# Kernel tuning notes

Hardware: AMD Instinct MI355X
Metric: run time of the kernel (lower is better)

## Reference

```python
import jax, jax.numpy as jnp
import numpy as np

B, N, NE = 16, 96, 256
ATOM, EDIM, HID, LAT, HEADS = 128, 16, 128, 128, 4
HD = LAT // HEADS
RBF, CUT, ZEMB, MAXZ = 16, 5.0, 32, 100
MUL0_IN, MUL1_IN = 64, 32      # irreps_node = 64x0e + 32x1o (dim 160)
MUL0_OUT, MUL1_OUT = 32, 16    # out irreps  = 32x0e + 16x1o (dim 80)
NODE_DIM = MUL0_IN + 3 * MUL1_IN
OUT_DIM = MUL0_OUT + 3 * MUL1_OUT
E_ATT = 1024
WNUM = MUL0_IN*MUL0_OUT + MUL0_IN*MUL1_OUT + MUL1_IN*MUL1_OUT + MUL1_IN*MUL0_OUT  # 4608


def _mlp3(x, w1, b1, w2, b2, w3, b3):
    x = jax.nn.silu(x @ w1 + b1)
    x = jax.nn.silu(x @ w2 + b2)
    return x @ w3 + b3


def setup_inputs() -> dict:
    key = jax.random.key(0)
    ks = jax.random.split(key, 40)
    s = 0.05  # scale params so deep MLP activations stay numerically sane
    d = {}
    d['h'] = jax.random.normal(ks[0], (B, N, ATOM), jnp.float32)
    d['h_full'] = jax.random.normal(ks[1], (B, N, NODE_DIM), jnp.float32)
    d['e_feat'] = jax.random.normal(ks[2], (NE, EDIM), jnp.float32)
    d['att_dist'] = jax.random.uniform(ks[3], (E_ATT,), jnp.float32)
    d['att_vec'] = jax.random.normal(ks[4], (E_ATT, 3), jnp.float32)
    d['z_emb_table'] = jax.random.normal(ks[5], (MAXZ + 1, ZEMB), jnp.float32) * s
    d['rw1'] = jax.random.normal(ks[6], (ZEMB + 1 + RBF, HID), jnp.float32) * s
    d['rb1'] = jnp.zeros((HID,), jnp.float32)
    d['rw2'] = jax.random.normal(ks[7], (HID, WNUM), jnp.float32) * s
    d['rb2'] = jnp.zeros((WNUM,), jnp.float32)
    d['ew1'] = jax.random.normal(ks[8], (EDIM, HID), jnp.float32) * s
    d['eb1'] = jnp.zeros((HID,), jnp.float32)
    d['ew2'] = jax.random.normal(ks[9], (HID, MUL0_OUT + MUL1_OUT), jnp.float32) * s
    d['eb2'] = jnp.zeros((MUL0_OUT + MUL1_OUT,), jnp.float32)
    d['qw1'] = jax.random.normal(ks[10], (ATOM + EDIM, HID), jnp.float32) * s
    d['qb1'] = jnp.zeros((HID,), jnp.float32)
    d['qw2'] = jax.random.normal(ks[11], (HID, HID), jnp.float32) * s
    d['qb2'] = jnp.zeros((HID,), jnp.float32)
    d['qw3'] = jax.random.normal(ks[12], (HID, LAT), jnp.float32) * s
    d['qb3'] = jnp.zeros((LAT,), jnp.float32)
    d['kw1'] = jax.random.normal(ks[13], (ATOM + ZEMB + 1 + RBF, HID), jnp.float32) * s
    d['kb1'] = jnp.zeros((HID,), jnp.float32)
    d['kw2'] = jax.random.normal(ks[14], (HID, HID), jnp.float32) * s
    d['kb2'] = jnp.zeros((HID,), jnp.float32)
    d['kw3'] = jax.random.normal(ks[15], (HID, LAT), jnp.float32) * s
    d['kb3'] = jnp.zeros((LAT,), jnp.float32)
    d['ow1'] = jax.random.normal(ks[16], (MUL0_OUT + MUL1_OUT, HID), jnp.float32) * s
    d['ob1'] = jnp.zeros((HID,), jnp.float32)
    d['ow2'] = jax.random.normal(ks[17], (HID, HID), jnp.float32) * s
    d['ob2'] = jnp.zeros((HID,), jnp.float32)
    d['ow3'] = jax.random.normal(ks[18], (HID, LAT), jnp.float32) * s
    d['ob3'] = jnp.zeros((LAT,), jnp.float32)
    d['z'] = jax.random.randint(ks[19], (B, N), 0, MAXZ)
    d['mask'] = jnp.ones((B, N), bool)
    d['absorber_index'] = jax.random.randint(ks[20], (B,), 0, N)
    d['att_dst'] = jnp.arange(E_ATT)  # unique flat indices into B*N
    return d


def reference(h, h_full, e_feat, att_dist, att_vec, z_emb_table,
              rw1, rb1, rw2, rb2, ew1, eb1, ew2, eb2,
              qw1, qb1, qw2, qb2, qw3, qb3,
              kw1, kb1, kw2, kb2, kw3, kb3,
              ow1, ob1, ow2, ob2, ow3, ob3,
              z, mask, absorber_index, att_dst):
    Bz, Na, Hd = h.shape
    F = Bz * Na
    nE = e_feat.shape[0]
    # scatter edge data into flat (B*N) atom slots
    am_flat = jnp.zeros((F,), bool).at[att_dst].set(True)
    d_flat = jnp.zeros((F,), h.dtype).at[att_dst].set(att_dist)
    v_flat = jnp.zeros((F, 3), h.dtype).at[att_dst].set(att_vec)
    att_mask = am_flat.reshape(Bz, Na) & mask
    # spherical harmonics (lmax=1, component normalization): Y0 = 1, Y1 = sqrt(3)*unit_vec
    un = v_flat / jnp.maximum(jnp.linalg.norm(v_flat, axis=-1, keepdims=True), 1e-8)
    y1 = jnp.sqrt(3.0) * un
    # Gaussian RBF on absorber->atom distance
    mu = jnp.linspace(0.0, CUT, RBF)
    delta = CUT / (RBF - 1)
    rbf = jnp.exp(-(d_flat[:, None] - mu) ** 2 / (2.0 * delta * delta))  # (F, RBF)
    zr = z_emb_table[z]                      # (B, N, ZEMB)
    zr_flat = zr.reshape(F, -1)
    is_abs = jnp.zeros((Bz, Na), h.dtype).at[jnp.arange(Bz), absorber_index].set(1.0)
    # radial MLP -> per-edge tensor-product weights
    w_in = jnp.concatenate([zr_flat, is_abs.reshape(F, 1), rbf], -1)
    tpw = jax.nn.silu(w_in @ rw1 + rb1) @ rw2 + rb2  # (F, WNUM)
    s1 = MUL0_IN * MUL0_OUT
    s2 = s1 + MUL0_IN * MUL1_OUT
    s3 = s2 + MUL1_IN * MUL1_OUT
    w00 = tpw[:, :s1].reshape(F, MUL0_IN, MUL0_OUT)   # 0e x 0e -> 0e
    w01 = tpw[:, s1:s2].reshape(F, MUL0_IN, MUL1_OUT) # 0e x 1o -> 1o
    w10 = tpw[:, s2:s3].reshape(F, MUL1_IN, MUL1_OUT) # 1o x 0e -> 1o
    w11 = tpw[:, s3:].reshape(F, MUL1_IN, MUL0_OUT)   # 1o x 1o -> 0e
    hf = h_full.reshape(F, -1)
    x0 = hf[:, :MUL0_IN]
    x1 = hf[:, MUL0_IN:].reshape(F, MUL1_IN, 3)
    alpha = 1.0 / jnp.sqrt(jnp.float32(MUL0_IN + MUL1_IN))  # path fan-in normalization
    c = 1.0 / jnp.sqrt(3.0)                                  # wigner-3j coeff for l=1 couplings
    out0 = alpha * (jnp.einsum('fi,fio->fo', x0, w00)
                    + c * jnp.einsum('fim,fm,fio->fo', x1, y1, w11))
    out1 = alpha * c * (jnp.einsum('fi,fm,fio->fom', x0, y1, w01)
                        + jnp.einsum('fim,fio->fom', x1, w10))
    v_irrep = jnp.concatenate([out0, out1.reshape(F, 3 * MUL1_OUT)], -1)  # (F, OUT_DIM)
    # cosine cutoff envelope + edge mask
    env = jnp.where(d_flat < CUT, 0.5 * (jnp.cos(jnp.pi * d_flat / CUT) + 1.0), 0.0)
    v_irrep = v_irrep * (am_flat.astype(h.dtype) * env)[:, None]
    # energy-conditioned per-irrep-channel modulation
    gates = jax.nn.silu(e_feat @ ew1 + eb1) @ ew2 + eb2  # (nE, 48)
    g_exp = jnp.concatenate([gates[:, :MUL0_OUT],
                             jnp.repeat(gates[:, MUL0_OUT:], 3, axis=-1)], -1)  # (nE, OUT_DIM)
    v_mod = (v_irrep[:, None, :] * g_exp[None]).reshape(Bz, Na, nE, OUT_DIM)
    # invariant multi-head scoring
    h_abs = h[jnp.arange(Bz), absorber_index]  # (B, H)
    q_in = jnp.concatenate([jnp.broadcast_to(h_abs[:, None], (Bz, nE, Hd)),
                            jnp.broadcast_to(e_feat[None], (Bz, nE, EDIM))], -1)
    q = _mlp3(q_in, qw1, qb1, qw2, qb2, qw3, qb3)  # (B, nE, LAT)
    atom_static = jnp.concatenate([h, zr, is_abs[..., None], rbf.reshape(Bz, Na, RBF)], -1)
    k = _mlp3(atom_static, kw1, kb1, kw2, kb2, kw3, kb3)  # (B, N, LAT)
    qh = q.reshape(Bz, nE, HEADS, HD)
    kh = k.reshape(Bz, Na, HEADS, HD)
    scores = (jnp.einsum('behd,bnhd->benh', qh, kh) * (HD ** -0.5)).mean(-1)  # (B, nE, N)
    m = att_mask[:, None, :]
    scores = jnp.where(m, scores, -1e9)
    attn = jax.nn.softmax(scores, axis=2) * m.astype(h.dtype)
    attn = attn / jnp.maximum(attn.sum(2, keepdims=True), 1e-8)
    out_irrep = jnp.einsum('ben,bnec->bec', attn, v_mod)  # (B, nE, OUT_DIM)
    # invariants: scalars + vector norms
    scal = out_irrep[..., :MUL0_OUT]
    vec = out_irrep[..., MUL0_OUT:].reshape(Bz, nE, MUL1_OUT, 3)
    inv = jnp.concatenate([scal, jnp.sqrt(jnp.sum(vec * vec, -1) + 1e-12)], -1)
    return _mlp3(inv, ow1, ob1, ow2, ob2, ow3, ob3)  # (B, nE, LAT)
```

## Files before the change

### kernel.cpp

```cpp
#include <hip/hip_runtime.h>
#include <hip/hip_fp16.h>
#include <math.h>

#define BB 16
#define NN 96
#define NE 256
#define FF (BB*NN)
#define ATOM 128
#define EDIM 16
#define HID 128
#define LAT 128
#define RBFN 16
#define CUTOFF 5.0f
#define ZEMB 32
#define E_ATT 1024
#define M0I 64
#define M1I 32
#define M0O 32
#define M1O 16
#define NODE_DIM 160
#define OUT_DIM 80
#define INVD 48
#define WNUM 4608

#define K1_TP 192
#define K1_EDGE_AT 192
#define K1_Q_AT 448
#define K1_GATE_AT 960
#define K1_PREP_AT 976
#define K1_BLKS 977

typedef _Float16 half8_t __attribute__((ext_vector_type(8)));
typedef float float4v __attribute__((ext_vector_type(4)));

__device__ __forceinline__ float silu_f(float x) { return x / (1.0f + expf(-x)); }

__global__ __launch_bounds__(256) void k1(
    const float* __restrict__ h, const float* __restrict__ h_full,
    const float* __restrict__ z_emb, const int* __restrict__ z,
    const int* __restrict__ absorber, const float* __restrict__ e_feat,
    const int* __restrict__ att_dst, const float* __restrict__ att_dist,
    const float* __restrict__ att_vec,
    const float* __restrict__ rw1, const float* __restrict__ rb1,
    const float* __restrict__ rw2, const float* __restrict__ rb2,
    const float* __restrict__ kw1, const float* __restrict__ kb1,
    const float* __restrict__ kw2, const float* __restrict__ kb2,
    const float* __restrict__ kw3, const float* __restrict__ kb3,
    const float* __restrict__ qw1, const float* __restrict__ qb1,
    const float* __restrict__ qw2, const float* __restrict__ qb2,
    const float* __restrict__ qw3, const float* __restrict__ qb3,
    const float* __restrict__ ew1, const float* __restrict__ eb1,
    const float* __restrict__ ew2, const float* __restrict__ eb2,
    float* __restrict__ kmatw, float* __restrict__ qmat,
    float* __restrict__ gexp, float* __restrict__ virr,
    int* __restrict__ inv)
{
    __shared__ __align__(16) char smemraw[21248];
    float* smem = (float*)smemraw;
    int blk = blockIdx.x;
    int t = threadIdx.x;

    if (blk < K1_TP) {
        __half* cS   = (__half*)smemraw;
        float*  winf = (float*)smemraw;
        float*  fbase = (float*)smemraw + 1088;
        float* x0f  = fbase;
        float* x1f  = fbase + 1024;
        float* xyf  = fbase + 2560;
        float* y1f  = fbase + 3072;
        float* envf = fbase + 3136;
        float* dS   = fbase + 3152;
        int*   fI   = (int*)(fbase + 3168);
        _Float16* hS = (_Float16*)(smemraw + 17088);

        int cls  = blk % 3;
        int tile = blk / 3;
        int e0t = tile * 16;
        if (t < 16) {
            int e = e0t + t;
            int f = att_dst[e];
            fI[t] = f;
            float d = att_dist[e];
            dS[t] = d;
            envf[t] = (d < CUTOFF) ? 0.5f*(cosf(3.14159265358979323846f*d/CUTOFF) + 1.0f) : 0.0f;
            float vx = att_vec[3*e], vy = att_vec[3*e+1], vz = att_vec[3*e+2];
            float nrm = sqrtf(vx*vx + vy*vy + vz*vz);
            float is = 1.0f / fmaxf(nrm, 1e-8f);
            const float s3 = 1.7320508075688772f;
            y1f[t*4]   = s3*vx*is;
            y1f[t*4+1] = s3*vy*is;
            y1f[t*4+2] = s3*vz*is;
        }
        __syncthreads();
        for (int u = t; u < 16*49; u += 256) {
            int e = u / 49, j = u - 49*(u/49);
            int f = fI[e];
            float v;
            if (j < ZEMB) v = z_emb[z[f]*ZEMB + j];
            else if (j == ZEMB) { int b = f / NN, nn = f - b*NN; v = (absorber[b] == nn) ? 1.0f : 0.0f; }
            else {
                int jr = j - 33;
                const float delta = CUTOFF / (RBFN - 1);
                float diff = dS[e] - jr*delta;
                v = expf(-diff*diff / (2.0f*delta*delta));
            }
            winf[e*52 + j] = v;
        }
        for (int p = 0; p < 10; p++) {
            int idx = t + 256*p;
            int edge = idx / 160, j = idx - 160*edge;
            float v = h_full[fI[edge]*NODE_DIM + j];
            if (j < M0I) x0f[edge*64 + j] = v;
            else         x1f[edge*96 + (j - M0I)] = v;
        }
        __syncthreads();
        for (int p = 0; p < 2; p++) {
            int idx = t + 256*p;
            int edge = idx >> 5, i = idx & 31;
            xyf[edge*32 + i] = x1f[edge*96 + 3*i]*y1f[edge*4]
                             + x1f[edge*96 + 3*i+1]*y1f[edge*4+1]
                             + x1f[edge*96 + 3*i+2]*y1f[edge*4+2];
        }
        {
            int e = t >> 4;
            const float* wf = winf + e*52;
            #pragma unroll
            for (int p = 0; p < 4; p++) {
                int c2 = 2*((t & 15) + 16*p);
                float2 a0 = *(const float2*)&rb1[c2];
                float2 a1 = make_float2(0.f, 0.f);
                #pragma unroll 8
                for (int i = 0; i < 48; i += 2) {
                    float x0v = wf[i], x1v = wf[i + 1];
                    float2 w0 = *(const float2*)&rw1[i*HID + c2];
                    float2 w1 = *(const float2*)&rw1[(i+1)*HID + c2];
                    a0.x += x0v*w0.x; a0.y += x0v*w0.y;
                    a1.x += x1v*w1.x; a1.y += x1v*w1.y;
                }
                {
                    float x0v = wf[48];
                    float2 w0 = *(const float2*)&rw1[48*HID + c2];
                    a0.x += x0v*w0.x; a0.y += x0v*w0.y;
                }
                *(__half2*)&hS[e*128 + c2] =
                    __floats2half2_rn(silu_f(a0.x + a1.x), silu_f(a0.y + a1.y));
            }
        }
        __syncthreads();

        int wv = t >> 6;
        int lane = t & 63;
        int mrow = lane & 15, quad = lane >> 4;
        half8_t af[4];
        #pragma unroll
        for (int kc = 0; kc < 4; kc++)
            af[kc] = *(const half8_t*)&hS[mrow*128 + quad*8 + kc*32];

        int edge = t >> 4, o = t & 15;
        float t00 = 0.f, t11 = 0.f;
        float t01 = 0.f, tm0 = 0.f, tm1 = 0.f, tm2 = 0.f;
        int clsAdd = (cls == 1) ? 1 : 0;

        for (int g = 0; g < 12; g++) {
            #pragma unroll
            for (int sub = 0; sub < 2; sub++) {
                int ntl = 2*wv + sub;
                int j = g*8 + ntl;
                int ntg = (cls == 2) ? (128 + j)
                                     : (2*j + clsAdd + ((j >= 64) ? 96 : 0));
                const float* bcol = rw2 + ntg*16 + mrow;
                float4v acc = {0.f, 0.f, 0.f, 0.f};
                #pragma unroll
                for (int kc = 0; kc < 4; kc++) {
                    half8_t bfr;
                    #pragma unroll
                    for (int m = 0; m < 8; m++)
                        bfr[m] = (_Float16)bcol[(quad*8 + kc*32 + m)*WNUM];
                    acc = __builtin_amdgcn_mfma_f32_16x16x32_f16(af[kc], bfr, acc, 0, 0, 0);
                }
                float bias = rb2[ntg*16 + mrow];
                #pragma unroll
                for (int r = 0; r < 4; r++)
                    cS[(quad*4 + r)*136 + ntl*16 + mrow] = __float2half(acc[r] + bias);
            }
            __syncthreads();
            const __half* cRow = cS + edge*136 + o;
            if (cls < 2) {
                if (g < 8) {
                    #pragma unroll
                    for (int nt = 0; nt < 8; nt++)
                        t00 += x0f[edge*64 + g*8 + nt]*__half2float(cRow[nt*16]);
                } else {
                    #pragma unroll
                    for (int nt = 0; nt < 8; nt++)
                        t11 += xyf[edge*32 + (g*8 + nt - 64)]*__half2float(cRow[nt*16]);
                }
            } else {
                if (g < 8) {
                    #pragma unroll
                    for (int nt = 0; nt < 8; nt++)
                        t01 += x0f[edge*64 + g*8 + nt]*__half2float(cRow[nt*16]);
                } else {
                    #pragma unroll
                    for (int nt = 0; nt < 8; nt++) {
                        int i = g*8 + nt - 64;
                        float C = __half2float(cRow[nt*16]);
                        tm0 += x1f[edge*96 + 3*i]*C;
                        tm1 += x1f[edge*96 + 3*i+1]*C;
                        tm2 += x1f[edge*96 + 3*i+2]*C;
                    }
                }
            }
            __syncthreads();
        }
        const float alpha = 0.10206207261596575f;
        const float ccf   = 0.5773502691896258f;
        int f = fI[edge];
        float env = envf[edge];
        if (cls < 2) {
            virr[f*OUT_DIM + cls*16 + o] = alpha*(t00 + ccf*t11)*env;
        } else {
            float y0 = y1f[edge*4], y1v = y1f[edge*4+1], y2 = y1f[edge*4+2];
            virr[f*OUT_DIM + M0O + 3*o]     = alpha*ccf*(t01*y0 + tm0)*env;
            virr[f*OUT_DIM + M0O + 3*o + 1] = alpha*ccf*(t01*y1v + tm1)*env;
            virr[f*OUT_DIM + M0O + 3*o + 2] = alpha*ccf*(t01*y2 + tm2)*env;
        }
    } else if (blk < K1_Q_AT) {
        float (*sin1)[184] = (float(*)[184])smem;
        float (*l1S)[128]  = (float(*)[128])(smem + 736);
        float (*l2S)[128]  = (float(*)[128])(smem + 736 + 512);
        int w = t >> 6;
        int c = t & 63;
        int e = (blk - K1_EDGE_AT)*4 + w;
        int f = att_dst[e];
        int b = f / NN, nn = f - b*NN;
        float d = att_dist[e];
        {
            float2 hv = *(const float2*)&h[f*ATOM + 2*c];
            sin1[w][2*c] = hv.x; sin1[w][2*c + 1] = hv.y;
        }
        if (c < ZEMB) sin1[w][ATOM + c] = z_emb[z[f]*ZEMB + c];
        if (c >= 32 && c < 48) {
            int j = c - 32;
            const float delta = CUTOFF / (RBFN - 1);
            float diff = d - j*delta;
            sin1[w][ATOM + ZEMB + 1 + j] = expf(-diff*diff / (2.0f*delta*delta));
        }
        if (c == 48) sin1[w][ATOM + ZEMB] = (absorber[b] == nn) ? 1.0f : 0.0f;
        __syncthreads();
        int c2 = 2*c;
        {
            float2 a0 = *(const float2*)&kb1[c2];
            float2 a1 = make_float2(0.f, 0.f);
            #pragma unroll 8
            for (int i = 0; i < 176; i += 2) {
                float x0v = sin1[w][i], x1v = sin1[w][i + 1];
                float2 w0 = *(const float2*)&kw1[i*HID + c2];
                float2 w1 = *(const float2*)&kw1[(i+1)*HID + c2];
                a0.x += x0v*w0.x; a0.y += x0v*w0.y;
                a1.x += x1v*w1.x; a1.y += x1v*w1.y;
            }
            {
                float x0v = sin1[w][176];
                float2 w0 = *(const float2*)&kw1[176*HID + c2];
                a0.x += x0v*w0.x; a0.y += x0v*w0.y;
            }
            l1S[w][c2] = silu_f(a0.x + a1.x); l1S[w][c2+1] = silu_f(a0.y + a1.y);
        }
        __syncthreads();
        {
            float2 a0 = *(const float2*)&kb2[c2];
            float2 a1 = make_float2(0.f, 0.f);
            #pragma unroll 8
            for (int i = 0; i < HID; i += 2) {
                float x0v = l1S[w][i], x1v = l1S[w][i + 1];
                float2 w0 = *(const float2*)&kw2[i*HID + c2];
                float2 w1 = *(const float2*)&kw2[(i+1)*HID + c2];
                a0.x += x0v*w0.x; a0.y += x0v*w0.y;
                a1.x += x1v*w1.x; a1.y += x1v*w1.y;
            }
            l2S[w][c2] = silu_f(a0.x + a1.x); l2S[w][c2+1] = silu_f(a0.y + a1.y);
        }
        __syncthreads();
        {
            float2 a0 = *(const float2*)&kb3[c2];
            float2 a1 = make_float2(0.f, 0.f);
            #pragma unroll 8
            for (int i = 0; i < HID; i += 2) {
                float x0v = l2S[w][i], x1v = l2S[w][i + 1];
                float2 w0 = *(const float2*)&kw3[i*HID + c2];
                float2 w1 = *(const float2*)&kw3[(i+1)*HID + c2];
                a0.x += x0v*w0.x; a0.y += x0v*w0.y;
                a1.x += x1v*w1.x; a1.y += x1v*w1.y;
            }
            float2 o; o.x = a0.x + a1.x; o.y = a0.y + a1.y;
            *(float2*)&kmatw[f*HID + c2] = o;
        }
    } else if (blk < K1_GATE_AT) {
        float* hA          = smem;
        float (*ef)[16]    = (float(*)[16])(smem + 128);
        float (*part)[128] = (float(*)[128])(smem + 256);
        float* l1S         = smem + 1280;
        float* l2S         = smem + 2304;
        int idx = blk - K1_Q_AT;
        int r0 = idx * 8;
        int b  = r0 >> 8;
        int e8 = r0 & 255;
        if (t < 32) *(float4*)&hA[t*4] = *(const float4*)&h[(b*NN + absorber[b])*ATOM + t*4];
        if (t >= 128 && t < 256) { int e = (t - 128) >> 4, j = t & 15; ef[e][j] = e_feat[(e8 + e)*EDIM + j]; }
        __syncthreads();
        int r = t >> 5, c0 = (t & 31)*4;
        {
            float4 a0 = make_float4(0,0,0,0);
            int k0 = r*16;
            #pragma unroll
            for (int k = 0; k < 16; k++) {
                float hv = hA[k0 + k];
                float4 w0 = *(const float4*)&qw1[(k0 + k)*HID + c0];
                a0.x += hv*w0.x; a0.y += hv*w0.y; a0.z += hv*w0.z; a0.w += hv*w0.w;
            }
            *(float4*)&part[r][c0] = a0;
        }
        __syncthreads();
        {
            float4 s = *(const float4*)&qb1[c0];
            #pragma unroll
            for (int g = 0; g < 8; g++) {
                float4 pg = *(const float4*)&part[g][c0];
                s.x += pg.x; s.y += pg.y; s.z += pg.z; s.w += pg.w;
            }
            #pragma unroll
            for (int j = 0; j < 16; j++) {
                float a = ef[r][j];
                float4 w0 = *(const float4*)&qw1[(ATOM + j)*HID + c0];
                s.x += a*w0.x; s.y += a*w0.y; s.z += a*w0.z; s.w += a*w0.w;
            }
            l1S[r*128 + c0]   = silu_f(s.x); l1S[r*128 + c0+1] = silu_f(s.y);
            l1S[r*128 + c0+2] = silu_f(s.z); l1S[r*128 + c0+3] = silu_f(s.w);
        }
        __syncthreads();
        {
            float4 a0 = *(const float4*)&qb2[c0];
            float4 a1 = make_float4(0,0,0,0);
            #pragma unroll 8
            for (int i = 0; i < HID; i += 2) {
                float x0v = l1S[r*128 + i], x1v = l1S[r*128 + i+1];
                float4 w0 = *(const float4*)&qw2[i*HID + c0];
                float4 w1 = *(const float4*)&qw2[(i+1)*HID + c0];
                a0.x += x0v*w0.x; a0.y += x0v*w0.y; a0.z += x0v*w0.z; a0.w += x0v*w0.w;
                a1.x += x1v*w1.x; a1.y += x1v*w1.y; a1.z += x1v*w1.z; a1.w += x1v*w1.w;
            }
            l2S[r*128 + c0]   = silu_f(a0.x + a1.x); l2S[r*128 + c0+1] = silu_f(a0.y + a1.y);
            l2S[r*128 + c0+2] = silu_f(a0.z + a1.z); l2S[r*128 + c0+3] = silu_f(a0.w + a1.w);
        }
        __syncthreads();
        {
            float4 a0 = *(const float4*)&qb3[c0];
            float4 a1 = make_float4(0,0,0,0);
            #pragma unroll 8
            for (int i = 0; i < HID; i += 2) {
                float x0v = l2S[r*128 + i], x1v = l2S[r*128 + i+1];
                float4 w0 = *(const float4*)&qw3[i*HID + c0];
                float4 w1 = *(const float4*)&qw3[(i+1)*HID + c0];
                a0.x += x0v*w0.x; a0.y += x0v*w0.y; a0.z += x0v*w0.z; a0.w += x0v*w0.w;
                a1.x += x1v*w1.x; a1.y += x1v*w1.y; a1.z += x1v*w1.z; a1.w += x1v*w1.w;
            }
            float4 o;
            o.x = a0.x + a1.x; o.y = a0.y + a1.y; o.z = a0.z + a1.z; o.w = a0.w + a1.w;
            *(float4*)&qmat[(r0 + r)*LAT + c0] = o;
        }
    } else if (blk < K1_PREP_AT) {
        float (*ef)[16]   = (float(*)[16])smem;
        float (*l1g)[128] = (float(*)[128])(smem + 256);
        float (*gg)[48]   = (float(*)[48])(smem + 256 + 2048);
        int e0 = (blk - K1_GATE_AT) * 16;
        { int e = t >> 4, i = t & 15; ef[e][i] = e_feat[(e0 + e)*EDIM + i]; }
        __syncthreads();
        int r = t >> 4, c0 = (t & 15)*8;
        {
            float4 a0 = *(const float4*)&eb1[c0];
            float4 a1 = *(const float4*)&eb1[c0 + 4];
            #pragma unroll
            for (int i = 0; i < EDIM; i++) {
                float a = ef[r][i];
                float4 w0 = *(const float4*)&ew1[i*HID + c0];
                float4 w1 = *(const float4*)&ew1[i*HID + c0 + 4];
                a0.x += a*w0.x; a0.y += a*w0.y; a0.z += a*w0.z; a0.w += a*w0.w;
                a1.x += a*w1.x; a1.y += a*w1.y; a1.z += a*w1.z; a1.w += a*w1.w;
            }
            l1g[r][c0]   = silu_f(a0.x); l1g[r][c0+1] = silu_f(a0.y);
            l1g[r][c0+2] = silu_f(a0.z); l1g[r][c0+3] = silu_f(a0.w);
            l1g[r][c0+4] = silu_f(a1.x); l1g[r][c0+5] = silu_f(a1.y);
            l1g[r][c0+6] = silu_f(a1.z); l1g[r][c0+7] = silu_f(a1.w);
        }
        __syncthreads();
        for (int u = t; u < 16*48; u += 256) {
            int e = u / 48, j = u - 48*(u/48);
            float acc = eb2[j];
            #pragma unroll 4
            for (int i = 0; i < HID; i++) acc += l1g[e][i]*ew2[i*48 + j];
            gg[e][j] = acc;
        }
        __syncthreads();
        for (int u = t; u < 16*80; u += 256) {
            int e = u / 80, cc = u - 80*(u/80);
            gexp[(e0 + e)*OUT_DIM + cc] = (cc < M0O) ? gg[e][cc] : gg[e][M0O + (cc - M0O)/3];
        }
    } else {
        for (int p = 0; p < 6; p++) inv[t + 256*p] = -1;
        __syncthreads();
        for (int p = 0; p < 4; p++) { int e = t + 256*p; inv[att_dst[e]] = e; }
    }
}

__global__ __launch_bounds__(256) void k_attf(
    const float* __restrict__ qmat, const float* __restrict__ kmat,
    const int* __restrict__ inv,
    const float* __restrict__ virr, const float* __restrict__ gexp,
    const float* __restrict__ ow1, const float* __restrict__ ob1,
    const float* __restrict__ ow2, const float* __restrict__ ob2,
    const float* __restrict__ ow3, const float* __restrict__ ob3,
    float* __restrict__ out)
{
    int b  = blockIdx.x >> 5;
    int e0 = (blockIdx.x & 31) * 8;
    int t = threadIdx.x;
    __shared__ float smem[16448];
    float (*aS)[100]   = (float(*)[100])smem;
    float (*gS)[84]    = (float(*)[84])(smem + 800);
    float (*ocS)[84]   = (float(*)[84])(smem + 1472);
    float* mS          = smem + 2144;
    float (*inS)[INVD] = (float(*)[INVD])(smem + 2240);
    float (*q8)[132]   = (float(*)[132])(smem + 2624);
    float* Kt          = smem + 3680;
    float (*l1S)[HID]  = (float(*)[HID])(smem + 3680);
    float (*l2S)[HID]  = (float(*)[HID])(smem + 3680 + 1024);

    if (t < 160) {
        int el = t / 20, c4 = t - 20*(t/20);
        *(float4*)&gS[el][c4*4] = *(const float4*)&gexp[(e0 + el)*OUT_DIM + c4*4];
    }
    if (t < NN) mS[t] = ((unsigned)inv[b*NN + t] < E_ATT) ? 1.0f : 0.0f;
    {
        int el = t >> 5, i4 = t & 31;
        *(float4*)&q8[el][i4*4] = *(const float4*)&qmat[(b*NE + e0 + el)*LAT + i4*4];
    }
    for (int p = 0; p < 12; p++) {
        int idx = t + 256*p; int n = idx >> 5, i4 = idx & 31;
        *(float4*)&Kt[n*133 + i4*4] = *(const float4*)&kmat[(b*NN + n)*LAT + i4*4];
    }
    __syncthreads();

    int el = t >> 5, tn = t & 31;
    float sacc0, sacc1, sacc2;
    {
        const float* qp = &q8[el][0];
        const float* kp0 = &Kt[tn*133];
        const float* kp1 = &Kt[(32 + tn)*133];
        const float* kp2 = &Kt[(64 + tn)*133];
        float a00 = 0.f, a01 = 0.f, a10 = 0.f, a11 = 0.f, a20 = 0.f, a21 = 0.f;
        #pragma unroll 16
        for (int i = 0; i < LAT; i += 2) {
            float q0 = qp[i], q1 = qp[i+1];
            a00 += q0*kp0[i]; a01 += q1*kp0[i+1];
            a10 += q0*kp1[i]; a11 += q1*kp1[i+1];
            a20 += q0*kp2[i]; a21 += q1*kp2[i+1];
        }
        sacc0 = a00 + a01; sacc1 = a10 + a11; sacc2 = a20 + a21;
    }

    {
        const float scale = 0.04419417382415922f;
        int ng = tn;
        float m0 = mS[ng], m1 = mS[ng + 32], m2 = mS[ng + 64];
        float s0 = (m0 != 0.f) ? sacc0*scale : -1e9f;
        float s1 = (m1 != 0.f) ? sacc1*scale : -1e9f;
        float s2 = (m2 != 0.f) ? sacc2*scale : -1e9f;
        float mx = fmaxf(s0, fmaxf(s1, s2));
        #pragma unroll
        for (int off = 1; off < 32; off <<= 1) mx = fmaxf(mx, __shfl_xor(mx, off));
        float e0v = expf(s0 - mx), e1v = expf(s1 - mx), e2v = expf(s2 - mx);
        float sm = e0v + e1v + e2v;
        #pragma unroll
        for (int off = 1; off < 32; off <<= 1) sm += __shfl_xor(sm, off);
        float r = 1.0f / sm;
        float p0 = m0*e0v*r, p1 = m1*e1v*r, p2 = m2*e2v*r;
        float ss = p0 + p1 + p2;
        #pragma unroll
        for (int off = 1; off < 32; off <<= 1) ss += __shfl_xor(ss, off);
        float is = 1.0f / fmaxf(ss, 1e-8f);
        aS[el][ng]      = p0*is;
        aS[el][ng + 32] = p1*is;
        aS[el][ng + 64] = p2*is;
    }
    __syncthreads();

    if (t < 160) {
        int el2 = t / 20, c4 = t - 20*(t/20);
        const float* vp = virr + (long)b*NN*OUT_DIM + c4*4;
        float4 acc = make_float4(0,0,0,0);
        #pragma unroll 8
        for (int n = 0; n < NN; n++) {
            float a = aS[el2][n];
            float4 v = *(const float4*)&vp[n*OUT_DIM];
            acc.x += a*v.x; acc.y += a*v.y; acc.z += a*v.z; acc.w += a*v.w;
        }
        float4 g = *(float4*)&gS[el2][c4*4];
        float4 o; o.x = acc.x*g.x; o.y = acc.y*g.y; o.z = acc.z*g.z; o.w = acc.w*g.w;
        *(float4*)&ocS[el2][c4*4] = o;
    }
    __syncthreads();

    for (int u = t; u < 8*INVD; u += 256) {
        int el2 = u / INVD, j = u - INVD*(u/INVD);
        float val;
        if (j < M0O) val = ocS[el2][j];
        else {
            int o = j - M0O;
            float x = ocS[el2][M0O + 3*o], y = ocS[el2][M0O + 3*o + 1], zz = ocS[el2][M0O + 3*o + 2];
            val = sqrtf(x*x + y*y + zz*zz + 1e-12f);
        }
        inS[el2][j] = val;
    }
    __syncthreads();

    int r = t >> 5, c0 = (t & 31)*4;
    {
        float4 a0 = *(const float4*)&ob1[c0];
        float4 a1 = make_float4(0,0,0,0);
        #pragma unroll 8
        for (int i = 0; i < INVD; i += 2) {
            float x0v = inS[r][i], x1v = inS[r][i+1];
            float4 w0 = *(const float4*)&ow1[i*HID + c0];
            float4 w1 = *(const float4*)&ow1[(i+1)*HID + c0];
            a0.x += x0v*w0.x; a0.y += x0v*w0.y; a0.z += x0v*w0.z; a0.w += x0v*w0.w;
            a1.x += x1v*w1.x; a1.y += x1v*w1.y; a1.z += x1v*w1.z; a1.w += x1v*w1.w;
        }
        l1S[r][c0]   = silu_f(a0.x + a1.x); l1S[r][c0+1] = silu_f(a0.y + a1.y);
        l1S[r][c0+2] = silu_f(a0.z + a1.z); l1S[r][c0+3] = silu_f(a0.w + a1.w);
    }
    __syncthreads();
    {
        float4 a0 = *(const float4*)&ob2[c0];
        float4 a1 = make_float4(0,0,0,0);
        #pragma unroll 8
        for (int i = 0; i < HID; i += 2) {
            float x0v = l1S[r][i], x1v = l1S[r][i+1];
            float4 w0 = *(const float4*)&ow2[i*HID + c0];
            float4 w1 = *(const float4*)&ow2[(i+1)*HID + c0];
            a0.x += x0v*w0.x; a0.y += x0v*w0.y; a0.z += x0v*w0.z; a0.w += x0v*w0.w;
            a1.x += x1v*w1.x; a1.y += x1v*w1.y; a1.z += x1v*w1.z; a1.w += x1v*w1.w;
        }
        l2S[r][c0]   = silu_f(a0.x + a1.x); l2S[r][c0+1] = silu_f(a0.y + a1.y);
        l2S[r][c0+2] = silu_f(a0.z + a1.z); l2S[r][c0+3] = silu_f(a0.w + a1.w);
    }
    __syncthreads();
    {
        float4 a0 = *(const float4*)&ob3[c0];
        float4 a1 = make_float4(0,0,0,0);
        #pragma unroll 8
        for (int i = 0; i < HID; i += 2) {
            float x0v = l2S[r][i], x1v = l2S[r][i+1];
            float4 w0 = *(const float4*)&ow3[i*HID + c0];
            float4 w1 = *(const float4*)&ow3[(i+1)*HID + c0];
            a0.x += x0v*w0.x; a0.y += x0v*w0.y; a0.z += x0v*w0.z; a0.w += x0v*w0.w;
            a1.x += x1v*w1.x; a1.y += x1v*w1.y; a1.z += x1v*w1.z; a1.w += x1v*w1.w;
        }
        float4 o;
        o.x = a0.x + a1.x; o.y = a0.y + a1.y; o.z = a0.z + a1.z; o.w = a0.w + a1.w;
        *(float4*)&out[((b*NE + e0) + r)*LAT + c0] = o;
    }
}

extern "C" void kernel_launch(void* const* d_in, const int* in_sizes, int n_in,
                              void* d_out, int out_size, void* d_ws, size_t ws_size,
                              hipStream_t stream) {
    const float* h        = (const float*)d_in[0];
    const float* h_full   = (const float*)d_in[1];
    const float* e_feat   = (const float*)d_in[2];
    const float* att_dist = (const float*)d_in[3];
    const float* att_vec  = (const float*)d_in[4];
    const float* z_emb    = (const float*)d_in[5];
    const float* rw1 = (const float*)d_in[6];  const float* rb1 = (const float*)d_in[7];
    const float* rw2 = (const float*)d_in[8];  const float* rb2 = (const float*)d_in[9];
    const float* ew1 = (const float*)d_in[10]; const float* eb1 = (const float*)d_in[11];
    const float* ew2 = (const float*)d_in[12]; const float* eb2 = (const float*)d_in[13];
    const float* qw1 = (const float*)d_in[14]; const float* qb1 = (const float*)d_in[15];
    const float* qw2 = (const float*)d_in[16]; const float* qb2 = (const float*)d_in[17];
    const float* qw3 = (const float*)d_in[18]; const float* qb3 = (const float*)d_in[19];
    const float* kw1 = (const float*)d_in[20]; const float* kb1 = (const float*)d_in[21];
    const float* kw2 = (const float*)d_in[22]; const float* kb2 = (const float*)d_in[23];
    const float* kw3 = (const float*)d_in[24]; const float* kb3 = (const float*)d_in[25];
    const float* ow1 = (const float*)d_in[26]; const float* ob1 = (const float*)d_in[27];
    const float* ow2 = (const float*)d_in[28]; const float* ob2 = (const float*)d_in[29];
    const float* ow3 = (const float*)d_in[30]; const float* ob3 = (const float*)d_in[31];
    const int* z        = (const int*)d_in[32];
    const int* absorber = (const int*)d_in[34];
    const int* att_dst  = (const int*)d_in[35];

    float* ws = (float*)d_ws;
    int*   inv     = (int*)ws;
    float* kmat    = ws + 5632;
    float* qmat    = ws + 202240;
    float* gexp    = ws + 726528;
    float* virr    = ws + 747008;

    float* out = (float*)d_out;

    k1<<<K1_BLKS, 256, 0, stream>>>(h, h_full, z_emb, z, absorber, e_feat,
                                    att_dst, att_dist, att_vec,
                                    rw1, rb1, rw2, rb2,
                                    kw1, kb1, kw2, kb2, kw3, kb3,
                                    qw1, qb1, qw2, qb2, qw3, qb3,
                                    ew1, eb1, ew2, eb2,
                                    kmat, qmat, gexp, virr, inv);
    k_attf<<<BB*32, 256, 0, stream>>>(qmat, kmat, inv, virr, gexp,
                                      ow1, ob1, ow2, ob2, ow3, ob3, out);
}
```

Baseline: 211.0 us.

## Contract MFMA outputs in registers, drop per-group LDS staging and barriers

The tensor-product section no longer writes each MFMA tile to a shared fp16 buffer and syncs twice per group. Each wave now owns a contiguous range of 24 weight columns and folds its MFMA accumulator directly into per-edge partial sums held in registers. A single cross-wave reduction through a new shared buffer produces the outputs. Padded strides (65/97/33) avoid LDS bank conflicts on the new column-wise reads. The cost is a larger LDS footprint (37760 bytes) that may cut occupancy. A side effect is that the fp16 rounding of intermediate coefficients is removed.

Result: no change. 211.3 us (+0.1%).

```diff
diff --git a/kernel.cpp b/kernel.cpp
--- a/kernel.cpp
+++ b/kernel.cpp
@@ -55,23 +55,23 @@
     float* __restrict__ gexp, float* __restrict__ virr,
     int* __restrict__ inv)
 {
-    __shared__ __align__(16) char smemraw[21248];
+    __shared__ __align__(16) char smemraw[37760];
     float* smem = (float*)smemraw;
     int blk = blockIdx.x;
     int t = threadIdx.x;
 
     if (blk < K1_TP) {
-        __half* cS   = (__half*)smemraw;
-        float*  winf = (float*)smemraw;
+        float*  winf  = (float*)smemraw;
         float*  fbase = (float*)smemraw + 1088;
         float* x0f  = fbase;
-        float* x1f  = fbase + 1024;
-        float* xyf  = fbase + 2560;
-        float* y1f  = fbase + 3072;
-        float* envf = fbase + 3136;
-        float* dS   = fbase + 3152;
-        int*   fI   = (int*)(fbase + 3168);
-        _Float16* hS = (_Float16*)(smemraw + 17088);
+        float* x1f  = fbase + 1040;
+        float* xyf  = fbase + 2592;
+        float* y1f  = fbase + 3120;
+        float* envf = fbase + 3184;
+        float* dS   = fbase + 3200;
+        int*   fI   = (int*)(fbase + 3216);
+        _Float16* hS = (_Float16*)(smemraw + 17280);
+        float* pS   = (float*)(smemraw + 21376);
 
         int cls  = blk % 3;
         int tile = blk / 3;
@@ -110,16 +110,16 @@
             int idx = t + 256*p;
             int edge = idx / 160, j = idx - 160*edge;
             float v = h_full[fI[edge]*NODE_DIM + j];
-            if (j < M0I) x0f[edge*64 + j] = v;
-            else         x1f[edge*96 + (j - M0I)] = v;
+            if (j < M0I) x0f[edge*65 + j] = v;
+            else         x1f[edge*97 + (j - M0I)] = v;
         }
         __syncthreads();
         for (int p = 0; p < 2; p++) {
             int idx = t + 256*p;
             int edge = idx >> 5, i = idx & 31;
-            xyf[edge*32 + i] = x1f[edge*96 + 3*i]*y1f[edge*4]
-                             + x1f[edge*96 + 3*i+1]*y1f[edge*4+1]
-                             + x1f[edge*96 + 3*i+2]*y1f[edge*4+2];
+            xyf[edge*33 + i] = x1f[edge*97 + 3*i]*y1f[edge*4]
+                             + x1f[edge*97 + 3*i+1]*y1f[edge*4+1]
+                             + x1f[edge*97 + 3*i+2]*y1f[edge*4+2];
         }
         {
             int e = t >> 4;
@@ -156,74 +156,86 @@
         for (int kc = 0; kc < 4; kc++)
             af[kc] = *(const half8_t*)&hS[mrow*128 + quad*8 + kc*32];
 
-        int edge = t >> 4, o = t & 15;
-        float t00 = 0.f, t11 = 0.f;
-        float t01 = 0.f, tm0 = 0.f, tm1 = 0.f, tm2 = 0.f;
         int clsAdd = (cls == 1) ? 1 : 0;
-
-        for (int g = 0; g < 12; g++) {
+        float pa[4] = {0.f,0.f,0.f,0.f}, pb[4] = {0.f,0.f,0.f,0.f};
+        float pc[4] = {0.f,0.f,0.f,0.f}, pd[4] = {0.f,0.f,0.f,0.f};
+
+        #pragma unroll 2
+        for (int jj = 0; jj < 24; jj++) {
+            int j = wv*24 + jj;
+            int ntg = (cls == 2) ? (128 + j)
+                                 : (2*j + clsAdd + ((j >= 64) ? 96 : 0));
+            const float* bcol = rw2 + ntg*16 + mrow;
+            float4v acc = {0.f, 0.f, 0.f, 0.f};
             #pragma unroll
-            for (int sub = 0; sub < 2; sub++) {
-                int ntl = 2*wv + sub;
-                int j = g*8 + ntl;
-                int ntg = (cls == 2) ? (128 + j)
-                                     : (2*j + clsAdd + ((j >= 64) ? 96 : 0));
-                const float* bcol = rw2 + ntg*16 + mrow;
-                float4v acc = {0.f, 0.f, 0.f, 0.f};
+            for (int kc = 0; kc < 4; kc++) {
+                half8_t bfr;
                 #pragma unroll
-                for (int kc = 0; kc < 4; kc++) {
-                    half8_t bfr;
+                for (int m = 0; m < 8; m++)
+                    bfr[m] = (_Float16)bcol[(quad*8 + kc*32 + m)*WNUM];
+                acc = __builtin_amdgcn_mfma_f32_16x16x32_f16(af[kc], bfr, acc, 0, 0, 0);
+            }
+            float bias = rb2[ntg*16 + mrow];
+            if (cls < 2) {
+                if (j < 64) {
                     #pragma unroll
-                    for (int m = 0; m < 8; m++)
-                        bfr[m] = (_Float16)bcol[(quad*8 + kc*32 + m)*WNUM];
-                    acc = __builtin_amdgcn_mfma_f32_16x16x32_f16(af[kc], bfr, acc, 0, 0, 0);
-                }
-                float bias = rb2[ntg*16 + mrow];
-                #pragma unroll
-                for (int r = 0; r < 4; r++)
-                    cS[(quad*4 + r)*136 + ntl*16 + mrow] = __float2half(acc[r] + bias);
-            }
-            __syncthreads();
-            const __half* cRow = cS + edge*136 + o;
-            if (cls < 2) {
-                if (g < 8) {
-                    #pragma unroll
-                    for (int nt = 0; nt < 8; nt++)
-                        t00 += x0f[edge*64 + g*8 + nt]*__half2float(cRow[nt*16]);
+                    for (int r = 0; r < 4; r++)
+                        pa[r] += x0f[(quad*4 + r)*65 + j]*(acc[r] + bias);
                 } else {
                     #pragma unroll
-                    for (int nt = 0; nt < 8; nt++)
-                        t11 += xyf[edge*32 + (g*8 + nt - 64)]*__half2float(cRow[nt*16]);
+                    for (int r = 0; r < 4; r++)
+                        pb[r] += xyf[(quad*4 + r)*33 + (j - 64)]*(acc[r] + bias);
                 }
             } else {
-                if (g < 8) {
+                if (j < 64) {
                     #pragma unroll
-                    for (int nt = 0; nt < 8; nt++)
-                        t01 += x0f[edge*64 + g*8 + nt]*__half2float(cRow[nt*16]);
+                    for (int r = 0; r < 4; r++)
+                        pa[r] += x0f[(quad*4 + r)*65 + j]*(acc[r] + bias);
                 } else {
+                    int i = j - 64;
                     #pragma unroll
-                    for (int nt = 0; nt < 8; nt++) {
-                        int i = g*8 + nt - 64;
-                        float C = __half2float(cRow[nt*16]);
-                        tm0 += x1f[edge*96 + 3*i]*C;
-                        tm1 += x1f[edge*96 + 3*i+1]*C;
-                        tm2 += x1f[edge*96 + 3*i+2]*C;
+                    for (int r = 0; r < 4; r++) {
+                        float C = acc[r] + bias;
+                        pb[r] += x1f[(quad*4 + r)*97 + 3*i]*C;
+                        pc[r] += x1f[(quad*4 + r)*97 + 3*i+1]*C;
+                        pd[r] += x1f[(quad*4 + r)*97 + 3*i+2]*C;
                     }
                 }
             }
-            __syncthreads();
-        }
-        const float alpha = 0.10206207261596575f;
-        const float ccf   = 0.5773502691896258f;
-        int f = fI[edge];
-        float env = envf[edge];
-        if (cls < 2) {
-            virr[f*OUT_DIM + cls*16 + o] = alpha*(t00 + ccf*t11)*env;
-        } else {
-            float y0 = y1f[edge*4], y1v = y1f[edge*4+1], y2 = y1f[edge*4+2];
-            virr[f*OUT_DIM + M0O + 3*o]     = alpha*ccf*(t01*y0 + tm0)*env;
-            virr[f*OUT_DIM + M0O + 3*o + 1] = alpha*ccf*(t01*y1v + tm1)*env;
-            virr[f*OUT_DIM + M0O + 3*o + 2] = alpha*ccf*(t01*y2 + tm2)*env;
+        }
+        #pragma unroll
+        for (int r = 0; r < 4; r++) {
+            int edge = quad*4 + r;
+            pS[((wv*4 + 0)*16 + edge)*16 + mrow] = pa[r];
+            pS[((wv*4 + 1)*16 + edge)*16 + mrow] = pb[r];
+            if (cls == 2) {
+                pS[((wv*4 + 2)*16 + edge)*16 + mrow] = pc[r];
+                pS[((wv*4 + 3)*16 + edge)*16 + mrow] = pd[r];
+            }
+        }
+        __syncthreads();
+        {
+            int edge = t >> 4, o = t & 15;
+            const float alpha = 0.10206207261596575f;
+            const float ccf   = 0.5773502691896258f;
+            int f = fI[edge];
+            float env = envf[edge];
+            float s0 = pS[((0*4+0)*16 + edge)*16 + o] + pS[((1*4+0)*16 + edge)*16 + o]
+                     + pS[((2*4+0)*16 + edge)*16 + o] + pS[((3*4+0)*16 + edge)*16 + o];
+            float s1 = pS[((0*4+1)*16 + edge)*16 + o] + pS[((1*4+1)*16 + edge)*16 + o]
+                     + pS[((2*4+1)*16 + edge)*16 + o] + pS[((3*4+1)*16 + edge)*16 + o];
+            if (cls < 2) {
+                virr[f*OUT_DIM + cls*16 + o] = alpha*(s0 + ccf*s1)*env;
+            } else {
+                float s2 = pS[((0*4+2)*16 + edge)*16 + o] + pS[((1*4+2)*16 + edge)*16 + o]
+                         + pS[((2*4+2)*16 + edge)*16 + o] + pS[((3*4+2)*16 + edge)*16 + o];
+                float s3 = pS[((0*4+3)*16 + edge)*16 + o] + pS[((1*4+3)*16 + edge)*16 + o]
+                         + pS[((2*4+3)*16 + edge)*16 + o] + pS[((3*4+3)*16 + edge)*16 + o];
+                float y0 = y1f[edge*4], y1v = y1f[edge*4+1], y2 = y1f[edge*4+2];
+                virr[f*OUT_DIM + M0O + 3*o]     = alpha*ccf*(s0*y0 + s1)*env;
+                virr[f*OUT_DIM + M0O + 3*o + 1] = alpha*ccf*(s0*y1v + s2)*env;
+                virr[f*OUT_DIM + M0O + 3*o + 2] = alpha*ccf*(s0*y2 + s3)*env;
+            }
         }
     } else if (blk < K1_Q_AT) {
         float (*sin1)[184] = (float(*)[184])smem;
```
